# Optimization experiments

Measured on AMD Instinct MI355X. Metric: run time of the kernel, lower is better.

Reference implementation:

```python
import jax, jax.numpy as jnp
import numpy as np

B, T, D = 4, 2048, 1024
E, K, F = 8, 2, 4096


def setup_inputs() -> dict:
    key = jax.random.key(0)
    ks = jax.random.split(key, 6)
    s = 0.02
    return {
        "x": jax.random.normal(ks[0], (B, T, D), dtype=jnp.float32),
        "gate_w": jax.random.normal(ks[1], (D, E), dtype=jnp.float32) * s,
        "w1": jax.random.normal(ks[2], (E, D, F), dtype=jnp.float32) * s,
        "b1": jax.random.normal(ks[3], (E, F), dtype=jnp.float32) * s,
        "w2": jax.random.normal(ks[4], (E, F, D), dtype=jnp.float32) * s,
        "b2": jax.random.normal(ks[5], (E, D), dtype=jnp.float32) * s,
    }


def reference(x, gate_w, w1, b1, w2, b2):
    b, t, d = x.shape
    xf = x.reshape(-1, d)                       # [N, D]
    logits = xf @ gate_w                        # [N, E]
    topv, topi = jax.lax.top_k(logits, K)       # [N, K]
    gates = jax.nn.softmax(topv, axis=-1)       # [N, K]
    # per-token per-expert combine weight (zero for unselected experts)
    onehot = jax.nn.one_hot(topi, E, dtype=xf.dtype)       # [N, K, E]
    comb = jnp.einsum('nk,nke->ne', gates, onehot)          # [N, E]
    out = jnp.zeros_like(xf)
    for e in range(E):  # small fixed expert loop; keeps [N,F] intermediate only
        h = jax.nn.gelu(xf @ w1[e] + b1[e], approximate=False)  # [N, F]
        y = h @ w2[e] + b2[e]                                   # [N, D]
        out = out + comb[:, e:e + 1] * y
    return out.reshape(b, t, d)
```

## Files before the change

### kernel.cpp

```cpp
#include <hip/hip_runtime.h>
#include <stdint.h>
#include <stddef.h>

#define N_TOK 8192
#define DIM   1024
#define NE    8
#define NF    4096
#define TM    128
#define TN    128
#define BKK   64
#define RCAP  (N_TOK*2 + NE*TM)
#define MAXMT (N_TOK/TM)

typedef __attribute__((ext_vector_type(8))) short short8;
typedef __attribute__((ext_vector_type(4))) float f32x4;

__device__ __forceinline__ float bf2f(short s){
  unsigned u = ((unsigned)(unsigned short)s) << 16;
  return __builtin_bit_cast(float, u);
}
__device__ __forceinline__ short f2bf(float f){
  unsigned u = __builtin_bit_cast(unsigned, f);
  u += 0x7fffu + ((u >> 16) & 1u);
  return (short)(u >> 16);
}

#define GLD_LDS16(g, l) __builtin_amdgcn_global_load_lds( \
    (const __attribute__((address_space(1))) void*)(g),   \
    (__attribute__((address_space(3))) void*)(l), 16, 0, 0)

__global__ __launch_bounds__(256) void gate_kernel(
    const float* __restrict__ x, const float* __restrict__ gw,
    int* __restrict__ topi, float* __restrict__ gatev, int* __restrict__ ctrl)
{
  int t = blockIdx.x * 4 + (threadIdx.x >> 6);
  int lane = threadIdx.x & 63;
  const float* xr = x + (size_t)t * DIM;
  float p[NE];
  #pragma unroll
  for (int e = 0; e < NE; e++) p[e] = 0.f;
  for (int i = lane; i < DIM; i += 64){
    float xv = xr[i];
    const float* g = gw + i * NE;
    #pragma unroll
    for (int e = 0; e < NE; e++) p[e] += xv * g[e];
  }
  #pragma unroll
  for (int off = 32; off > 0; off >>= 1){
    #pragma unroll
    for (int e = 0; e < NE; e++) p[e] += __shfl_xor(p[e], off, 64);
  }
  if (lane == 0){
    int i1 = 0; float v1 = p[0];
    #pragma unroll
    for (int e = 1; e < NE; e++) if (p[e] > v1){ v1 = p[e]; i1 = e; }
    int i2 = -1; float v2 = -3.4e38f;
    #pragma unroll
    for (int e = 0; e < NE; e++) if (e != i1 && p[e] > v2){ v2 = p[e]; i2 = e; }
    float ex = expf(v2 - v1);
    float g2 = ex / (1.f + ex);
    float g1 = 1.f - g2;
    topi[t*2]   = i1;  topi[t*2+1]  = i2;
    gatev[t*2]  = g1;  gatev[t*2+1] = g2;
    atomicAdd(&ctrl[i1], 1);
    atomicAdd(&ctrl[i2], 1);
  }
}

__global__ void scan_kernel(int* ctrl){
  if (threadIdx.x == 0){
    int tot = 0;
    for (int e = 0; e < NE; e++){
      int c = ctrl[e];
      int cap = (c + TM - 1) & ~(TM - 1);
      ctrl[16+e] = tot; ctrl[24+e] = cap; tot += cap;
    }
  }
}

__global__ __launch_bounds__(256) void scatter_kernel(
    const int* __restrict__ topi, int* ctrl,
    int* __restrict__ rowTok, int* __restrict__ tok2row)
{
  int t = blockIdx.x * 256 + threadIdx.x;
  #pragma unroll
  for (int k = 0; k < 2; k++){
    int e = topi[t*2 + k];
    int pos = atomicAdd(&ctrl[8+e], 1);
    int r = ctrl[16+e] + pos;
    rowTok[r] = t;
    tok2row[t*2 + k] = r;
  }
}

__global__ void pad_kernel(const int* __restrict__ ctrl, int* __restrict__ rowTok){
  int e = blockIdx.x;
  int cnt = ctrl[e], cap = ctrl[24+e], off = ctrl[16+e];
  for (int i = cnt + threadIdx.x; i < cap; i += blockDim.x)
    rowTok[off + i] = N_TOK;
}

__global__ __launch_bounds__(256) void cast_x_kernel(
    const float* __restrict__ x, short* __restrict__ xb)
{
  size_t i = ((size_t)blockIdx.x * 256 + threadIdx.x) * 8;
  if (i >= (size_t)(N_TOK + 1) * DIM) return;
  short8 o;
  if (i < (size_t)N_TOK * DIM){
    #pragma unroll
    for (int j = 0; j < 8; j++) o[j] = f2bf(x[i + j]);
  } else {
    #pragma unroll
    for (int j = 0; j < 8; j++) o[j] = 0;
  }
  *(short8*)(xb + i) = o;
}

__global__ __launch_bounds__(256) void cast_w_kernel(
    const float* __restrict__ src, short* __restrict__ dst, int Kd, int Nd)
{
  long tid = (long)blockIdx.x * 256 + threadIdx.x;
  int within = (int)(tid & 1023);
  long tile = tid >> 10;
  int nn = within & 127;
  int ko = within >> 7;
  int kt = Kd / 64;
  int kb = (int)(tile % kt); long tmp = tile / kt;
  int nb = (int)(tmp % (Nd / 128)); int e = (int)(tmp / (Nd / 128));
  const float* s = src + (size_t)e * Kd * Nd;
  short8 o;
  #pragma unroll
  for (int j = 0; j < 8; j++){
    int k = kb*64 + ko*8 + j;
    int n = nb*128 + nn;
    o[j] = f2bf(s[(size_t)k * Nd + n]);
  }
  *(short8*)(dst + tile*8192 + nn*64 + ko*8) = o;
}

__global__ __launch_bounds__(256) void ffn1_kernel(
    const short* __restrict__ Xb, const short* __restrict__ W1s,
    const float* __restrict__ b1, const int* __restrict__ ctrl,
    const int* __restrict__ rowTok, short* __restrict__ H)
{
  int e = blockIdx.z, mt = blockIdx.y, nb = blockIdx.x;
  int cap = ctrl[24+e];
  if (mt * TM >= cap) return;
  int rowbase = ctrl[16+e] + mt * TM;

  __shared__ __align__(16) short As[TM][BKK];
  __shared__ __align__(16) short Bs[TN][BKK];

  int tid = threadIdx.x, w = tid >> 6, lane = tid & 63;
  int rsub = lane >> 3, ksub = lane & 7;

  const short* ap[4];
  #pragma unroll
  for (int j = 0; j < 4; j++){
    int g = rowTok[rowbase + w*32 + j*8 + rsub];
    ap[j] = Xb + (size_t)g * DIM + ksub * 8;
  }
  const short* btile = W1s + ((size_t)(e * (NF/TN) + nb) * (DIM/BKK)) * (TN*BKK);
  const short* bp[4];
  #pragma unroll
  for (int j = 0; j < 4; j++) bp[j] = btile + ((w*4 + j)*64 + lane) * 8;

  char* AsB = (char*)As; char* BsB = (char*)Bs;
  int ml = lane & 15, q = lane >> 4;
  int wm = w & 1, wn = w >> 1;
  const short8* Ar = (const short8*)As;
  const short8* Br = (const short8*)Bs;

  f32x4 acc[4][4];
  #pragma unroll
  for (int i = 0; i < 4; i++){
    #pragma unroll
    for (int j = 0; j < 4; j++){ f32x4 z = {0.f,0.f,0.f,0.f}; acc[i][j] = z; }
  }

  for (int kb = 0; kb < DIM/BKK; kb++){
    #pragma unroll
    for (int j = 0; j < 4; j++) GLD_LDS16(ap[j] + kb*BKK, AsB + (w*4 + j)*1024);
    #pragma unroll
    for (int j = 0; j < 4; j++) GLD_LDS16(bp[j] + kb*(TN*BKK), BsB + (w*4 + j)*1024);
    __syncthreads();
    #pragma unroll
    for (int ks = 0; ks < 2; ks++){
      short8 a[4], b[4];
      #pragma unroll
      for (int mi = 0; mi < 4; mi++) a[mi] = Ar[(wm*64 + mi*16 + ml)*8 + ks*4 + q];
      #pragma unroll
      for (int ni = 0; ni < 4; ni++) b[ni] = Br[(wn*64 + ni*16 + ml)*8 + ks*4 + q];
      #pragma unroll
      for (int mi = 0; mi < 4; mi++){
        #pragma unroll
        for (int ni = 0; ni < 4; ni++)
          acc[mi][ni] = __builtin_amdgcn_mfma_f32_16x16x32_bf16(a[mi], b[ni], acc[mi][ni], 0, 0, 0);
      }
    }
    __syncthreads();
  }

  #pragma unroll
  for (int ni = 0; ni < 4; ni++){
    int f = nb*TN + wn*64 + ni*16 + ml;
    float bb = b1[e*NF + f];
    #pragma unroll
    for (int mi = 0; mi < 4; mi++){
      #pragma unroll
      for (int r = 0; r < 4; r++){
        int m = wm*64 + mi*16 + q*4 + r;
        float v = acc[mi][ni][r] + bb;
        float h = 0.5f * v * (1.f + erff(v * 0.70710678118654752f));
        H[(size_t)(rowbase + m) * NF + f] = f2bf(h);
      }
    }
  }
}

__global__ __launch_bounds__(256) void ffn2_kernel(
    const short* __restrict__ H, const short* __restrict__ W2s,
    const float* __restrict__ b2, const int* __restrict__ ctrl,
    short* __restrict__ Yp)
{
  int e = blockIdx.z, mt = blockIdx.y, nb = blockIdx.x;
  int cap = ctrl[24+e];
  if (mt * TM >= cap) return;
  int rowbase = ctrl[16+e] + mt * TM;

  __shared__ __align__(16) short As[TM][BKK];
  __shared__ __align__(16) short Bs[TN][BKK];

  int tid = threadIdx.x, w = tid >> 6, lane = tid & 63;
  int rsub = lane >> 3, ksub = lane & 7;

  const short* ap[4];
  #pragma unroll
  for (int j = 0; j < 4; j++){
    int r = rowbase + w*32 + j*8 + rsub;
    ap[j] = H + (size_t)r * NF + ksub * 8;
  }
  const short* btile = W2s + ((size_t)(e * (DIM/TN) + nb) * (NF/BKK)) * (TN*BKK);
  const short* bp[4];
  #pragma unroll
  for (int j = 0; j < 4; j++) bp[j] = btile + ((w*4 + j)*64 + lane) * 8;

  char* AsB = (char*)As; char* BsB = (char*)Bs;
  int ml = lane & 15, q = lane >> 4;
  int wm = w & 1, wn = w >> 1;
  const short8* Ar = (const short8*)As;
  const short8* Br = (const short8*)Bs;

  f32x4 acc[4][4];
  #pragma unroll
  for (int i = 0; i < 4; i++){
    #pragma unroll
    for (int j = 0; j < 4; j++){ f32x4 z = {0.f,0.f,0.f,0.f}; acc[i][j] = z; }
  }

  for (int kb = 0; kb < NF/BKK; kb++){
    #pragma unroll
    for (int j = 0; j < 4; j++) GLD_LDS16(ap[j] + kb*BKK, AsB + (w*4 + j)*1024);
    #pragma unroll
    for (int j = 0; j < 4; j++) GLD_LDS16(bp[j] + kb*(TN*BKK), BsB + (w*4 + j)*1024);
    __syncthreads();
    #pragma unroll
    for (int ks = 0; ks < 2; ks++){
      short8 a[4], b[4];
      #pragma unroll
      for (int mi = 0; mi < 4; mi++) a[mi] = Ar[(wm*64 + mi*16 + ml)*8 + ks*4 + q];
      #pragma unroll
      for (int ni = 0; ni < 4; ni++) b[ni] = Br[(wn*64 + ni*16 + ml)*8 + ks*4 + q];
      #pragma unroll
      for (int mi = 0; mi < 4; mi++){
        #pragma unroll
        for (int ni = 0; ni < 4; ni++)
          acc[mi][ni] = __builtin_amdgcn_mfma_f32_16x16x32_bf16(a[mi], b[ni], acc[mi][ni], 0, 0, 0);
      }
    }
    __syncthreads();
  }

  #pragma unroll
  for (int ni = 0; ni < 4; ni++){
    int d = nb*TN + wn*64 + ni*16 + ml;
    float bb = b2[e*DIM + d];
    #pragma unroll
    for (int mi = 0; mi < 4; mi++){
      #pragma unroll
      for (int r = 0; r < 4; r++){
        int m = wm*64 + mi*16 + q*4 + r;
        Yp[(size_t)(rowbase + m) * DIM + d] = f2bf(acc[mi][ni][r] + bb);
      }
    }
  }
}

__global__ __launch_bounds__(256) void combine_kernel(
    const short* __restrict__ Yp, const int* __restrict__ tok2row,
    const float* __restrict__ gatev, float* __restrict__ out)
{
  int idx = blockIdx.x * 256 + threadIdx.x;
  int t = idx >> 7, d8 = idx & 127;
  int r0 = tok2row[t*2], r1 = tok2row[t*2 + 1];
  float g0 = gatev[t*2], g1 = gatev[t*2 + 1];
  short8 y0 = *(const short8*)(Yp + (size_t)r0 * DIM + d8*8);
  short8 y1 = *(const short8*)(Yp + (size_t)r1 * DIM + d8*8);
  float o[8];
  #pragma unroll
  for (int j = 0; j < 8; j++) o[j] = g0 * bf2f(y0[j]) + g1 * bf2f(y1[j]);
  f32x4 v0 = {o[0], o[1], o[2], o[3]};
  f32x4 v1 = {o[4], o[5], o[6], o[7]};
  f32x4* dst = (f32x4*)(out + (size_t)t * DIM + d8*8);
  dst[0] = v0; dst[1] = v1;
}

extern "C" void kernel_launch(void* const* d_in, const int* in_sizes, int n_in,
                              void* d_out, int out_size, void* d_ws, size_t ws_size,
                              hipStream_t stream)
{
  const float* x  = (const float*)d_in[0];
  const float* gw = (const float*)d_in[1];
  const float* w1 = (const float*)d_in[2];
  const float* b1 = (const float*)d_in[3];
  const float* w2 = (const float*)d_in[4];
  const float* b2 = (const float*)d_in[5];
  float* out = (float*)d_out;

  char* ws = (char*)d_ws;
  size_t o = 0;
  int*   ctrl    = (int*)(ws + o); o += 256;
  int*   topi    = (int*)(ws + o); o += (size_t)N_TOK*2*4;
  float* gatev   = (float*)(ws + o); o += (size_t)N_TOK*2*4;
  int*   rowTok  = (int*)(ws + o); o += (size_t)RCAP*4;
  int*   tok2row = (int*)(ws + o); o += (size_t)N_TOK*2*4;
  o = (o + 255) & ~(size_t)255;
  short* Xb  = (short*)(ws + o); o += (size_t)(N_TOK + 1)*DIM*2;
  short* W1s = (short*)(ws + o); o += (size_t)NE*DIM*NF*2;
  short* W2s = (short*)(ws + o); o += (size_t)NE*NF*DIM*2;
  short* H   = (short*)(ws + o); o += (size_t)RCAP*NF*2;
  short* Yp  = (short*)(ws + o); o += (size_t)RCAP*DIM*2;
  (void)in_sizes; (void)n_in; (void)out_size;

  if (o > ws_size) return;

  hipMemsetAsync(ctrl, 0, 256, stream);
  gate_kernel<<<N_TOK/4, 256, 0, stream>>>(x, gw, topi, gatev, ctrl);
  scan_kernel<<<1, 64, 0, stream>>>(ctrl);
  scatter_kernel<<<N_TOK/256, 256, 0, stream>>>(topi, ctrl, rowTok, tok2row);
  pad_kernel<<<NE, 128, 0, stream>>>(ctrl, rowTok);
  cast_x_kernel<<<((N_TOK + 1)*DIM/8 + 255)/256, 256, 0, stream>>>(x, Xb);
  cast_w_kernel<<<NE*(NF/128)*(DIM/64)*1024/256, 256, 0, stream>>>(w1, W1s, DIM, NF);
  cast_w_kernel<<<NE*(DIM/128)*(NF/64)*1024/256, 256, 0, stream>>>(w2, W2s, NF, DIM);
  ffn1_kernel<<<dim3(NF/TN, MAXMT, NE), 256, 0, stream>>>(Xb, W1s, b1, ctrl, rowTok, H);
  ffn2_kernel<<<dim3(DIM/TN, MAXMT, NE), 256, 0, stream>>>(H, W2s, b2, ctrl, Yp);
  combine_kernel<<<N_TOK*(DIM/8)/256, 256, 0, stream>>>(Yp, tok2row, gatev, out);
}
```

Before: 1.288 ms.

## Transpose weights via LDS and XOR-swizzle GEMM shared-memory tiles

Replaces the strided weight cast kernel with an LDS-staged transpose-cast that reads fp32 weights coalesced and writes them N-major (row per output column, contiguous K). The FFN GEMMs now load B rows from this plain transposed layout and apply an XOR swizzle on the 16-byte chunk index for both A and B tiles, on the global-to-LDS load and again on the fragment reads, to avoid LDS bank conflicts. This targets uncoalesced reads in the weight conversion and bank conflicts in the MFMA inner loop. The trade-off is that B-tile global loads become row-strided instead of fully contiguous per tile.

```diff
diff --git a/kernel.cpp b/kernel.cpp
--- a/kernel.cpp
+++ b/kernel.cpp
@@ -116,30 +116,35 @@
   *(short8*)(xb + i) = o;
 }
 
-__global__ __launch_bounds__(256) void cast_w_kernel(
+__global__ __launch_bounds__(256) void transpose_cast_kernel(
     const float* __restrict__ src, short* __restrict__ dst, int Kd, int Nd)
 {
-  long tid = (long)blockIdx.x * 256 + threadIdx.x;
-  int within = (int)(tid & 1023);
-  long tile = tid >> 10;
-  int nn = within & 127;
-  int ko = within >> 7;
-  int kt = Kd / 64;
-  int kb = (int)(tile % kt); long tmp = tile / kt;
-  int nb = (int)(tmp % (Nd / 128)); int e = (int)(tmp / (Nd / 128));
+  __shared__ float Ls[64][65];
+  int e = blockIdx.z;
+  int k0 = blockIdx.y * 64, n0 = blockIdx.x * 64;
   const float* s = src + (size_t)e * Kd * Nd;
-  short8 o;
-  #pragma unroll
-  for (int j = 0; j < 8; j++){
-    int k = kb*64 + ko*8 + j;
-    int n = nb*128 + nn;
-    o[j] = f2bf(s[(size_t)k * Nd + n]);
-  }
-  *(short8*)(dst + tile*8192 + nn*64 + ko*8) = o;
+  short*       d = dst + (size_t)e * Kd * Nd;
+  int t = threadIdx.x;
+  int kr = t >> 4, nc = (t & 15) * 4;
+  #pragma unroll
+  for (int rr = 0; rr < 4; rr++){
+    int k = rr*16 + kr;
+    f32x4 v = *(const f32x4*)(s + (size_t)(k0 + k) * Nd + n0 + nc);
+    Ls[k][nc+0] = v[0]; Ls[k][nc+1] = v[1];
+    Ls[k][nc+2] = v[2]; Ls[k][nc+3] = v[3];
+  }
+  __syncthreads();
+  int nr = t >> 2, kc = (t & 3) * 16;
+  short o[16];
+  #pragma unroll
+  for (int i = 0; i < 16; i++) o[i] = f2bf(Ls[kc + i][nr]);
+  short* dp = d + (size_t)(n0 + nr) * Kd + k0 + kc;
+  *(short8*)(dp)     = *(short8*)&o[0];
+  *(short8*)(dp + 8) = *(short8*)&o[8];
 }
 
 __global__ __launch_bounds__(256) void ffn1_kernel(
-    const short* __restrict__ Xb, const short* __restrict__ W1s,
+    const short* __restrict__ Xb, const short* __restrict__ W1t,
     const float* __restrict__ b1, const int* __restrict__ ctrl,
     const int* __restrict__ rowTok, short* __restrict__ H)
 {
@@ -153,21 +158,24 @@
 
   int tid = threadIdx.x, w = tid >> 6, lane = tid & 63;
   int rsub = lane >> 3, ksub = lane & 7;
+  int sw = (ksub ^ rsub) * 8;
 
   const short* ap[4];
   #pragma unroll
   for (int j = 0; j < 4; j++){
     int g = rowTok[rowbase + w*32 + j*8 + rsub];
-    ap[j] = Xb + (size_t)g * DIM + ksub * 8;
-  }
-  const short* btile = W1s + ((size_t)(e * (NF/TN) + nb) * (DIM/BKK)) * (TN*BKK);
+    ap[j] = Xb + (size_t)g * DIM + sw;
+  }
+  const short* bbase = W1t + ((size_t)e * NF + (size_t)nb * TN) * DIM;
   const short* bp[4];
   #pragma unroll
-  for (int j = 0; j < 4; j++) bp[j] = btile + ((w*4 + j)*64 + lane) * 8;
+  for (int j = 0; j < 4; j++)
+    bp[j] = bbase + (size_t)((w*4 + j)*8 + rsub) * DIM + sw;
 
   char* AsB = (char*)As; char* BsB = (char*)Bs;
   int ml = lane & 15, q = lane >> 4;
   int wm = w & 1, wn = w >> 1;
+  int mx = ml & 7;
   const short8* Ar = (const short8*)As;
   const short8* Br = (const short8*)Bs;
 
@@ -182,15 +190,16 @@
     #pragma unroll
     for (int j = 0; j < 4; j++) GLD_LDS16(ap[j] + kb*BKK, AsB + (w*4 + j)*1024);
     #pragma unroll
-    for (int j = 0; j < 4; j++) GLD_LDS16(bp[j] + kb*(TN*BKK), BsB + (w*4 + j)*1024);
+    for (int j = 0; j < 4; j++) GLD_LDS16(bp[j] + kb*BKK, BsB + (w*4 + j)*1024);
     __syncthreads();
     #pragma unroll
     for (int ks = 0; ks < 2; ks++){
+      int c = (ks*4 + q) ^ mx;
       short8 a[4], b[4];
       #pragma unroll
-      for (int mi = 0; mi < 4; mi++) a[mi] = Ar[(wm*64 + mi*16 + ml)*8 + ks*4 + q];
-      #pragma unroll
-      for (int ni = 0; ni < 4; ni++) b[ni] = Br[(wn*64 + ni*16 + ml)*8 + ks*4 + q];
+      for (int mi = 0; mi < 4; mi++) a[mi] = Ar[(wm*64 + mi*16 + ml)*8 + c];
+      #pragma unroll
+      for (int ni = 0; ni < 4; ni++) b[ni] = Br[(wn*64 + ni*16 + ml)*8 + c];
       #pragma unroll
       for (int mi = 0; mi < 4; mi++){
         #pragma unroll
@@ -219,7 +228,7 @@
 }
 
 __global__ __launch_bounds__(256) void ffn2_kernel(
-    const short* __restrict__ H, const short* __restrict__ W2s,
+    const short* __restrict__ H, const short* __restrict__ W2t,
     const float* __restrict__ b2, const int* __restrict__ ctrl,
     short* __restrict__ Yp)
 {
@@ -233,21 +242,24 @@
 
   int tid = threadIdx.x, w = tid >> 6, lane = tid & 63;
   int rsub = lane >> 3, ksub = lane & 7;
+  int sw = (ksub ^ rsub) * 8;
 
   const short* ap[4];
   #pragma unroll
   for (int j = 0; j < 4; j++){
     int r = rowbase + w*32 + j*8 + rsub;
-    ap[j] = H + (size_t)r * NF + ksub * 8;
-  }
-  const short* btile = W2s + ((size_t)(e * (DIM/TN) + nb) * (NF/BKK)) * (TN*BKK);
+    ap[j] = H + (size_t)r * NF + sw;
+  }
+  const short* bbase = W2t + ((size_t)e * DIM + (size_t)nb * TN) * NF;
   const short* bp[4];
   #pragma unroll
-  for (int j = 0; j < 4; j++) bp[j] = btile + ((w*4 + j)*64 + lane) * 8;
+  for (int j = 0; j < 4; j++)
+    bp[j] = bbase + (size_t)((w*4 + j)*8 + rsub) * NF + sw;
 
   char* AsB = (char*)As; char* BsB = (char*)Bs;
   int ml = lane & 15, q = lane >> 4;
   int wm = w & 1, wn = w >> 1;
+  int mx = ml & 7;
   const short8* Ar = (const short8*)As;
   const short8* Br = (const short8*)Bs;
 
@@ -262,15 +274,16 @@
     #pragma unroll
     for (int j = 0; j < 4; j++) GLD_LDS16(ap[j] + kb*BKK, AsB + (w*4 + j)*1024);
     #pragma unroll
-    for (int j = 0; j < 4; j++) GLD_LDS16(bp[j] + kb*(TN*BKK), BsB + (w*4 + j)*1024);
+    for (int j = 0; j < 4; j++) GLD_LDS16(bp[j] + kb*BKK, BsB + (w*4 + j)*1024);
     __syncthreads();
     #pragma unroll
     for (int ks = 0; ks < 2; ks++){
+      int c = (ks*4 + q) ^ mx;
       short8 a[4], b[4];
       #pragma unroll
-      for (int mi = 0; mi < 4; mi++) a[mi] = Ar[(wm*64 + mi*16 + ml)*8 + ks*4 + q];
-      #pragma unroll
-      for (int ni = 0; ni < 4; ni++) b[ni] = Br[(wn*64 + ni*16 + ml)*8 + ks*4 + q];
+      for (int mi = 0; mi < 4; mi++) a[mi] = Ar[(wm*64 + mi*16 + ml)*8 + c];
+      #pragma unroll
+      for (int ni = 0; ni < 4; ni++) b[ni] = Br[(wn*64 + ni*16 + ml)*8 + c];
       #pragma unroll
       for (int mi = 0; mi < 4; mi++){
         #pragma unroll
@@ -336,8 +349,8 @@
   int*   tok2row = (int*)(ws + o); o += (size_t)N_TOK*2*4;
   o = (o + 255) & ~(size_t)255;
   short* Xb  = (short*)(ws + o); o += (size_t)(N_TOK + 1)*DIM*2;
-  short* W1s = (short*)(ws + o); o += (size_t)NE*DIM*NF*2;
-  short* W2s = (short*)(ws + o); o += (size_t)NE*NF*DIM*2;
+  short* W1t = (short*)(ws + o); o += (size_t)NE*DIM*NF*2;
+  short* W2t = (short*)(ws + o); o += (size_t)NE*NF*DIM*2;
   short* H   = (short*)(ws + o); o += (size_t)RCAP*NF*2;
   short* Yp  = (short*)(ws + o); o += (size_t)RCAP*DIM*2;
   (void)in_sizes; (void)n_in; (void)out_size;
@@ -350,9 +363,9 @@
   scatter_kernel<<<N_TOK/256, 256, 0, stream>>>(topi, ctrl, rowTok, tok2row);
   pad_kernel<<<NE, 128, 0, stream>>>(ctrl, rowTok);
   cast_x_kernel<<<((N_TOK + 1)*DIM/8 + 255)/256, 256, 0, stream>>>(x, Xb);
-  cast_w_kernel<<<NE*(NF/128)*(DIM/64)*1024/256, 256, 0, stream>>>(w1, W1s, DIM, NF);
-  cast_w_kernel<<<NE*(DIM/128)*(NF/64)*1024/256, 256, 0, stream>>>(w2, W2s, NF, DIM);
-  ffn1_kernel<<<dim3(NF/TN, MAXMT, NE), 256, 0, stream>>>(Xb, W1s, b1, ctrl, rowTok, H);
-  ffn2_kernel<<<dim3(DIM/TN, MAXMT, NE), 256, 0, stream>>>(H, W2s, b2, ctrl, Yp);
+  transpose_cast_kernel<<<dim3(NF/64, DIM/64, NE), 256, 0, stream>>>(w1, W1t, DIM, NF);
+  transpose_cast_kernel<<<dim3(DIM/64, NF/64, NE), 256, 0, stream>>>(w2, W2t, NF, DIM);
+  ffn1_kernel<<<dim3(NF/TN, MAXMT, NE), 256, 0, stream>>>(Xb, W1t, b1, ctrl, rowTok, H);
+  ffn2_kernel<<<dim3(DIM/TN, MAXMT, NE), 256, 0, stream>>>(H, W2t, b2, ctrl, Yp);
   combine_kernel<<<N_TOK*(DIM/8)/256, 256, 0, stream>>>(Yp, tok2row, gatev, out);
 }
```

New measurement: 1.124 ms. -12.7%, faster.
